# Kernel tuning notes

Hardware: AMD Instinct MI355X
Metric: run time of the kernel (lower is better)

## Reference

```python
import jax, jax.numpy as jnp
import numpy as np

EPS = 1e-5
NUM_GRAPHS = 64


def _linear(x, W, b):
    return x @ W + b


def setup_inputs() -> dict:
    key = jax.random.key(0)
    ks = jax.random.split(key, 32)
    N, E, IN, EF, H, ED, T, L, C = 25000, 400000, 128, 16, 32, 32, 4, 2, 1
    F = H            # F_in (divide_input=False)
    Fo = H // T      # F_out per tower

    def w(k, shape):
        return jax.random.normal(k, shape, jnp.float32) / np.sqrt(shape[-2])

    inp = {
        'x': jax.random.normal(ks[0], (N, IN), jnp.float32),
        'edge_attr': jax.random.normal(ks[1], (E, EF), jnp.float32),
        'edge_weight': jax.random.uniform(ks[2], (E,), jnp.float32),
        'edge_index': jax.random.randint(ks[3], (2, E), 0, N),
        'batch': jnp.sort(jax.random.randint(ks[4], (N,), 0, NUM_GRAPHS)),
        'node_W': w(ks[5], (IN, H)), 'node_b': jnp.zeros((H,), jnp.float32),
        'edge_W': w(ks[6], (EF, ED)), 'edge_b': jnp.zeros((ED,), jnp.float32),
        'enc_W': w(ks[7], (L, ED, F)), 'enc_b': jnp.zeros((L, F), jnp.float32),
        'pre_W': w(ks[8], (L, T, 3 * F, F)), 'pre_b': jnp.zeros((L, T, F), jnp.float32),
        'post_W': w(ks[9], (L, T, 13 * F, Fo)), 'post_b': jnp.zeros((L, T, Fo), jnp.float32),
        'lin_W': w(ks[10], (L, H, H)), 'lin_b': jnp.zeros((L, H), jnp.float32),
        'bn_g': jnp.ones((L, H), jnp.float32), 'bn_b': jnp.zeros((L, H), jnp.float32),
        'mlp_W1': w(ks[11], (H, H)), 'mlp_b1': jnp.zeros((H,), jnp.float32),
        'mlp_W2': w(ks[12], (H, H // 2)), 'mlp_b2': jnp.zeros((H // 2,), jnp.float32),
        'mlp_W3': w(ks[13], (H // 2, C)), 'mlp_b3': jnp.zeros((C,), jnp.float32),
    }
    return inp


def reference(x, edge_attr, edge_weight, node_W, node_b, edge_W, edge_b,
              enc_W, enc_b, pre_W, pre_b, post_W, post_b, lin_W, lin_b,
              bn_g, bn_b, mlp_W1, mlp_b1, mlp_W2, mlp_b2, mlp_W3, mlp_b3,
              edge_index, batch):
    N = x.shape[0]
    L, T = pre_W.shape[0], pre_W.shape[1]
    src, dst = edge_index[0], edge_index[1]

    # degree-based scalers (PNA): avg_deg_log = mean_n log(deg_n + 1)
    deg = jax.ops.segment_sum(jnp.ones((src.shape[0],), x.dtype), dst, num_segments=N)
    avg_deg_log = jnp.mean(jnp.log(deg + 1.0))
    degc = jnp.clip(deg, 1.0)[:, None, None]          # [N,1,1]
    log_deg = jnp.log(degc + 1.0)
    amp = log_deg / avg_deg_log                        # amplification scaler
    att = avg_deg_log / log_deg                        # attenuation scaler
    has_edge = (deg > 0)[:, None, None]

    h = _linear(x, node_W, node_b)                     # node_emb  [N,H]
    e = _linear(edge_attr, edge_W, edge_b)             # edge_emb  [E,ED]

    for l in range(L):
        el = _linear(e, enc_W[l], enc_b[l])            # edge_encoder [E,F]
        m_in = jnp.concatenate([h[dst], h[src], el], axis=-1)      # [E,3F]
        msg = jnp.einsum('ef,tfg->etg', m_in, pre_W[l]) + pre_b[l]  # per-tower pre_nn [E,T,F]
        msg = msg * edge_weight[:, None, None]
        s = jax.ops.segment_sum(msg, dst, num_segments=N)
        s2 = jax.ops.segment_sum(msg * msg, dst, num_segments=N)
        mean = s / degc
        std = jnp.sqrt(jax.nn.relu(s2 / degc - mean * mean) + EPS)
        mn = jnp.where(has_edge, jax.ops.segment_min(msg, dst, num_segments=N), 0.0)
        mx = jnp.where(has_edge, jax.ops.segment_max(msg, dst, num_segments=N), 0.0)
        agg = jnp.concatenate([mean, mn, mx, std], axis=-1)            # [N,T,4F]
        agg = jnp.concatenate([agg, agg * amp, agg * att], axis=-1)    # [N,T,12F]
        out = jnp.concatenate(
            [jnp.broadcast_to(h[:, None, :], (N, T, h.shape[-1])), agg], axis=-1)  # [N,T,13F]
        out = jnp.einsum('ntf,tfg->ntg', out, post_W[l]) + post_b[l]   # post_nn [N,T,Fo]
        out = out.reshape(N, -1) @ lin_W[l] + lin_b[l]                 # [N,H]
        mu = jnp.mean(out, axis=0)
        var = jnp.var(out, axis=0)
        out = (out - mu) / jnp.sqrt(var + EPS) * bn_g[l] + bn_b[l]     # BatchNorm (batch stats)
        h = jax.nn.relu(out)

    g = jax.ops.segment_sum(h, batch, num_segments=NUM_GRAPHS)        # global_add_pool
    g = jax.nn.relu(_linear(g, mlp_W1, mlp_b1))
    g = jax.nn.relu(_linear(g, mlp_W2, mlp_b2))
    return _linear(g, mlp_W3, mlp_b3)
```

## Files before the change

### kernel.cpp

```cpp
#include <hip/hip_runtime.h>

constexpr float kEps = 1e-5f;

__device__ __forceinline__ unsigned short f2bf(float x) {
  unsigned int u = __float_as_uint(x);
  unsigned int r = (u + 0x7fffu + ((u >> 16) & 1u)) >> 16;
  return (unsigned short)r;
}
__device__ __forceinline__ float bflo(unsigned int u) { return __uint_as_float(u << 16); }
__device__ __forceinline__ float bfhi(unsigned int u) { return __uint_as_float(u & 0xffff0000u); }
__device__ __forceinline__ unsigned int packbf(float a, float b) {
  return (unsigned int)f2bf(a) | ((unsigned int)f2bf(b) << 16);
}


__global__ void zero_int2(int* __restrict__ a, int* __restrict__ b, int n) {
  int i = blockIdx.x * blockDim.x + threadIdx.x;
  if (i < n) { a[i] = 0; b[i] = 0; }
}

__global__ void hist_kernel(const int* __restrict__ dst, int* __restrict__ deg, int E) {
  int e = blockIdx.x * blockDim.x + threadIdx.x;
  if (e < E) atomicAdd(&deg[dst[e]], 1);
}

__global__ void scan1_kernel(const int* __restrict__ deg, int* __restrict__ off,
                             int* __restrict__ part, int N) {
  __shared__ int sm[1024];
  int i = blockIdx.x * 1024 + threadIdx.x;
  int v = (i < N) ? deg[i] : 0;
  sm[threadIdx.x] = v;
  __syncthreads();
  for (int o = 1; o < 1024; o <<= 1) {
    int t = (threadIdx.x >= o) ? sm[threadIdx.x - o] : 0;
    __syncthreads();
    sm[threadIdx.x] += t;
    __syncthreads();
  }
  if (i < N) off[i] = sm[threadIdx.x] - v;
  if (threadIdx.x == 1023) part[blockIdx.x] = sm[1023];
}

__global__ void scan2_kernel(int* __restrict__ part, int* __restrict__ off, int nb, int N) {
  if (threadIdx.x == 0) {
    int run = 0;
    for (int b = 0; b < nb; b++) { int p = part[b]; part[b] = run; run += p; }
    off[N] = run;
  }
}

__global__ void scan3_kernel(int* __restrict__ off, const int* __restrict__ part, int N) {
  int i = blockIdx.x * 1024 + threadIdx.x;
  if (i < N) off[i] += part[blockIdx.x];
}

__global__ void fill_kernel(const int* __restrict__ src, const int* __restrict__ dst,
                            const float* __restrict__ ew, const int* __restrict__ off,
                            int* __restrict__ cnt, int* __restrict__ edg,
                            int* __restrict__ srcs, float* __restrict__ ews, int E) {
  int e = blockIdx.x * blockDim.x + threadIdx.x;
  if (e < E) {
    int d = dst[e];
    int slot = off[d] + atomicAdd(&cnt[d], 1);
    edg[slot] = e;
    srcs[slot] = src[e];
    ews[slot] = ew[e];
  }
}

__global__ void egather_kernel(const int* __restrict__ edg, const float4* __restrict__ eattr4,
                               float4* __restrict__ eattrg4, int E4) {
  int i = blockIdx.x * blockDim.x + threadIdx.x;
  if (i < E4) {
    int slot = i >> 2, quad = i & 3;
    int e = edg[slot];
    eattrg4[i] = eattr4[e * 4 + quad];
  }
}

__global__ void adl_kernel(const int* __restrict__ deg, float* __restrict__ adl, int N) {
  __shared__ float sm[1024];
  float s = 0.f;
  for (int n = threadIdx.x; n < N; n += 1024) s += logf((float)deg[n] + 1.f);
  sm[threadIdx.x] = s;
  __syncthreads();
  for (int o = 512; o > 0; o >>= 1) {
    if (threadIdx.x < o) sm[threadIdx.x] += sm[threadIdx.x + o];
    __syncthreads();
  }
  if (threadIdx.x == 0) adl[0] = sm[0];
}

__global__ void node_emb_kernel(const float* __restrict__ x, const float* __restrict__ W,
                                const float* __restrict__ b, float* __restrict__ h, int N) {
  int n = blockIdx.x * 8 + (threadIdx.x >> 5);
  int j = threadIdx.x & 31;
  if (n >= N) return;
  float acc = b[j];
  const float4* x4 = (const float4*)(x + (size_t)n * 128);
#pragma unroll
  for (int q = 0; q < 32; q++) {
    float4 v = x4[q];
    acc += v.x * W[(4 * q + 0) * 32 + j];
    acc += v.y * W[(4 * q + 1) * 32 + j];
    acc += v.z * W[(4 * q + 2) * 32 + j];
    acc += v.w * W[(4 * q + 3) * 32 + j];
  }
  h[n * 32 + j] = acc;
}

__global__ void fuse_kernel(const float* __restrict__ edge_W, const float* __restrict__ edge_b,
                            const float* __restrict__ enc_W, const float* __restrict__ enc_b,
                            const float* __restrict__ pre_W, const float* __restrict__ pre_b,
                            float* __restrict__ Wf, float* __restrict__ bf) {
  __shared__ float tW[2][16][32];
  __shared__ float tb[2][32];
  int tid = threadIdx.x;
  for (int i = tid; i < 1024; i += 256) {
    int l = i >> 9, r = (i >> 5) & 15, c = i & 31;
    float s = 0.f;
    for (int k = 0; k < 32; k++) s += edge_W[r * 32 + k] * enc_W[(l * 32 + k) * 32 + c];
    tW[l][r][c] = s;
  }
  for (int i = tid; i < 64; i += 256) {
    int l = i >> 5, c = i & 31;
    float s = enc_b[l * 32 + c];
    for (int k = 0; k < 32; k++) s += edge_b[k] * enc_W[(l * 32 + k) * 32 + c];
    tb[l][c] = s;
  }
  __syncthreads();
  for (int i = tid; i < 4096; i += 256) {
    int l = i >> 11, t = (i >> 9) & 3, r = (i >> 5) & 15, c = i & 31;
    float s = 0.f;
    for (int k = 0; k < 32; k++) s += tW[l][r][k] * pre_W[((l * 4 + t) * 96 + 64 + k) * 32 + c];
    Wf[i] = s;
  }
  for (int i = tid; i < 256; i += 256) {
    int l = i >> 7, t = (i >> 5) & 3, c = i & 31;
    float s = pre_b[(l * 4 + t) * 32 + c];
    for (int k = 0; k < 32; k++) s += tb[l][k] * pre_W[((l * 4 + t) * 96 + 64 + k) * 32 + c];
    bf[i] = s;
  }
}

__global__ __launch_bounds__(256) void prep_kernel(
    const float* __restrict__ h, const float* __restrict__ preW,
    const float* __restrict__ bfv, unsigned short* __restrict__ qB,
    unsigned short* __restrict__ AB, float* __restrict__ bn, int N) {
  if (blockIdx.x == 0 && threadIdx.x < 64) bn[threadIdx.x] = 0.f;
  __shared__ float hs[16][32];
  int tid = threadIdx.x;
  int c = tid & 127, half = tid >> 7;
  int t = c >> 5, g = c & 31;
  float ws[32], wd[32];
  {
    const float* pS = preW + (t * 96 + 32) * 32 + g;
    const float* pD = preW + (t * 96) * 32 + g;
#pragma unroll
    for (int k = 0; k < 32; k++) { ws[k] = pS[k * 32]; wd[k] = pD[k * 32]; }
  }
  float bc = bfv[c];
  int base = blockIdx.x * 16;
  for (int i = tid; i < 512; i += 256) {
    int nn = i >> 5;
    hs[nn][i & 31] = (base + nn < N) ? h[(size_t)(base + nn) * 32 + (i & 31)] : 0.f;
  }
  __syncthreads();
#pragma unroll
  for (int nn = 0; nn < 8; ++nn) {
    int nl = half + 2 * nn;
    int n = base + nl;
    if (n >= N) continue;
    float qa = 0.f, Aa = bc;
#pragma unroll
    for (int k = 0; k < 32; k++) {
      float hk = hs[nl][k];
      qa = fmaf(hk, ws[k], qa);
      Aa = fmaf(hk, wd[k], Aa);
    }
    qB[(size_t)n * 128 + c] = f2bf(qa);
    AB[(size_t)n * 128 + c] = f2bf(Aa);
  }
}

#define FOLD8(F0, F1, VA, VB, O)                                           \
  F0 = fmaf(VA.x, wfa[O + 0], F0); F1 = fmaf(VA.x, wfb[O + 0], F1);        \
  F0 = fmaf(VA.y, wfa[O + 1], F0); F1 = fmaf(VA.y, wfb[O + 1], F1);        \
  F0 = fmaf(VA.z, wfa[O + 2], F0); F1 = fmaf(VA.z, wfb[O + 2], F1);        \
  F0 = fmaf(VA.w, wfa[O + 3], F0); F1 = fmaf(VA.w, wfb[O + 3], F1);        \
  F0 = fmaf(VB.x, wfa[O + 4], F0); F1 = fmaf(VB.x, wfb[O + 4], F1);        \
  F0 = fmaf(VB.y, wfa[O + 5], F0); F1 = fmaf(VB.y, wfb[O + 5], F1);        \
  F0 = fmaf(VB.z, wfa[O + 6], F0); F1 = fmaf(VB.z, wfb[O + 6], F1);        \
  F0 = fmaf(VB.w, wfa[O + 7], F0); F1 = fmaf(VB.w, wfb[O + 7], F1);

#define STATACC(V0, V1)                                                    \
  s0a += V0; sq0 = fmaf(V0, V0, sq0); mn0 = fminf(mn0, V0); mx0 = fmaxf(mx0, V0); \
  s1a += V1; sq1 = fmaf(V1, V1, sq1); mn1 = fminf(mn1, V1); mx1 = fmaxf(mx1, V1);

__global__ __launch_bounds__(256, 4) void agg3_kernel(
    const unsigned int* __restrict__ qB, const unsigned int* __restrict__ AB,
    const int* __restrict__ coff, const int* __restrict__ srcs,
    const float* __restrict__ ews, const float* __restrict__ eattrg,
    const float* __restrict__ Wf, unsigned int* __restrict__ stats, int N) {
  int lane = threadIdx.x & 63;
  int n = (blockIdx.x * blockDim.x + threadIdx.x) >> 6;
  if (n >= N) return;
  int t = lane >> 4, g0 = (2 * lane) & 31;
  float wfa[16], wfb[16];
  {
    const float* p = Wf + t * 512 + g0;
#pragma unroll
    for (int k = 0; k < 16; k++) { wfa[k] = p[k * 32]; wfb[k] = p[k * 32 + 1]; }
  }
  unsigned int au = AB[(size_t)n * 64 + lane];
  float a0 = bflo(au), a1 = bfhi(au);
  int beg = coff[n], end = coff[n + 1];
  int dg = end - beg;
  float s0a = 0.f, s1a = 0.f, sq0 = 0.f, sq1 = 0.f;
  float mn0 = 1e30f, mn1 = 1e30f, mx0 = -1e30f, mx1 = -1e30f;

  int i = beg;
  int sc0 = 0, sc1 = 0, sc2 = 0, sc3 = 0;
  if (i + 4 <= end) { sc0 = srcs[i]; sc1 = srcs[i + 1]; sc2 = srcs[i + 2]; sc3 = srcs[i + 3]; }
  for (; i + 4 <= end; i += 4) {
    unsigned int q0 = qB[(size_t)sc0 * 64 + lane];
    unsigned int q1 = qB[(size_t)sc1 * 64 + lane];
    unsigned int q2 = qB[(size_t)sc2 * 64 + lane];
    unsigned int q3 = qB[(size_t)sc3 * 64 + lane];
    float w0 = ews[i], w1 = ews[i + 1], w2 = ews[i + 2], w3 = ews[i + 3];
    const float4* ep = (const float4*)(eattrg + (size_t)i * 16);
    if (i + 8 <= end) { sc0 = srcs[i + 4]; sc1 = srcs[i + 5]; sc2 = srcs[i + 6]; sc3 = srcs[i + 7]; }
    float f00 = 0.f, f10 = 0.f, f01 = 0.f, f11 = 0.f;
    float f02 = 0.f, f12 = 0.f, f03 = 0.f, f13 = 0.f;
    {
      float4 aA = ep[0], aB = ep[1], bA = ep[4], bB = ep[5];
      float4 cA = ep[8], cB = ep[9], dA = ep[12], dB = ep[13];
      FOLD8(f00, f10, aA, aB, 0)
      FOLD8(f01, f11, bA, bB, 0)
      FOLD8(f02, f12, cA, cB, 0)
      FOLD8(f03, f13, dA, dB, 0)
    }
    {
      float4 aA = ep[2], aB = ep[3], bA = ep[6], bB = ep[7];
      float4 cA = ep[10], cB = ep[11], dA = ep[14], dB = ep[15];
      FOLD8(f00, f10, aA, aB, 8)
      FOLD8(f01, f11, bA, bB, 8)
      FOLD8(f02, f12, cA, cB, 8)
      FOLD8(f03, f13, dA, dB, 8)
    }
    float v0, v1;
    v0 = (a0 + bflo(q0) + f00) * w0; v1 = (a1 + bfhi(q0) + f10) * w0; STATACC(v0, v1)
    v0 = (a0 + bflo(q1) + f01) * w1; v1 = (a1 + bfhi(q1) + f11) * w1; STATACC(v0, v1)
    v0 = (a0 + bflo(q2) + f02) * w2; v1 = (a1 + bfhi(q2) + f12) * w2; STATACC(v0, v1)
    v0 = (a0 + bflo(q3) + f03) * w3; v1 = (a1 + bfhi(q3) + f13) * w3; STATACC(v0, v1)
  }
  for (; i < end; ++i) {
    int s = srcs[i];
    unsigned int q = qB[(size_t)s * 64 + lane];
    float w = ews[i];
    const float4* ep = (const float4*)(eattrg + (size_t)i * 16);
    float4 aA = ep[0], aB = ep[1], cA = ep[2], cB = ep[3];
    float f0 = 0.f, f1 = 0.f;
    FOLD8(f0, f1, aA, aB, 0)
    FOLD8(f0, f1, cA, cB, 8)
    float v0 = (a0 + bflo(q) + f0) * w;
    float v1 = (a1 + bfhi(q) + f1) * w;
    STATACC(v0, v1)
  }
  if (dg == 0) { mn0 = 0.f; mx0 = 0.f; mn1 = 0.f; mx1 = 0.f; }
  float inv = 1.f / (float)(dg > 0 ? dg : 1);
  float mean0 = s0a * inv, mean1 = s1a * inv;
  float sd0 = sqrtf(fmaxf(sq0 * inv - mean0 * mean0, 0.f) + kEps);
  float sd1 = sqrtf(fmaxf(sq1 * inv - mean1 * mean1, 0.f) + kEps);
  unsigned int* sp = stats + (size_t)n * 256;
  sp[0 * 64 + lane] = packbf(mean0, mean1);
  sp[1 * 64 + lane] = packbf(mn0, mn1);
  sp[2 * 64 + lane] = packbf(mx0, mx1);
  sp[3 * 64 + lane] = packbf(sd0, sd1);
}

__global__ __launch_bounds__(256) void post_kernel(
    const float* __restrict__ h, const unsigned int* __restrict__ stats,
    const int* __restrict__ coff, const float* __restrict__ adl,
    const float* __restrict__ postW, const float* __restrict__ postB,
    const float* __restrict__ linW, const float* __restrict__ linB,
    float* __restrict__ pre, float* __restrict__ bn, int N) {
  __shared__ unsigned int pwp[208 * 32];
  __shared__ unsigned int stu[4][256];
  __shared__ float red[8][32];
  int tid = threadIdx.x;
  for (int i = tid; i < 6656; i += 256) {
    int r = i >> 5, cc = i & 31, tP = cc >> 3, gq = cc & 7;
    float lo = postW[tP * 3328 + (2 * r) * 8 + gq];
    float hi = postW[tP * 3328 + (2 * r + 1) * 8 + gq];
    pwp[i] = packbf(lo, hi);
  }
  __syncthreads();

  int wave = tid >> 6, lane = tid & 63;
  int c = lane & 31, hh = lane >> 5;
  int tP = c >> 3;
  float adN = adl[0];
  float bs = 0.f, bq = 0.f;

  for (int n = blockIdx.x * 4 + wave; n < N; n += gridDim.x * 4) {
    {
      uint4 su = ((const uint4*)stats)[(size_t)n * 64 + lane];
      ((uint4*)stu[wave])[lane] = su;
    }
    int dg = coff[n + 1] - coff[n];
    float degc = (float)(dg > 0 ? dg : 1);
    float ad = adN / (float)N;
    float ld = logf(degc + 1.f);
    float amp = ld / ad, att = ad / ld;

    float acc = (hh == 0) ? postB[tP * 8 + (c & 7)] : 0.f;
    const float4* h4 = (const float4*)(h + (size_t)n * 32);
#pragma unroll
    for (int q4 = 0; q4 < 4; q4++) {
      float4 hv = h4[hh * 4 + q4];
      int r0 = hh * 8 + q4 * 2;
      unsigned int u0 = pwp[r0 * 32 + c], u1 = pwp[(r0 + 1) * 32 + c];
      acc = fmaf(hv.x, bflo(u0), acc);
      acc = fmaf(hv.y, bfhi(u0), acc);
      acc = fmaf(hv.z, bflo(u1), acc);
      acc = fmaf(hv.w, bfhi(u1), acc);
    }
#pragma unroll 8
    for (int jj = 0; jj < 32; jj++) {
      int sIdx = hh * 2 + (jj >> 4);
      unsigned int sv = stu[wave][sIdx * 64 + tP * 16 + (jj & 15)];
      float v0 = bflo(sv), v1 = bfhi(sv);
      int rm = 16 + hh * 32 + jj, ra = 80 + hh * 32 + jj, rt = 144 + hh * 32 + jj;
      unsigned int um = pwp[rm * 32 + c];
      unsigned int ua = pwp[ra * 32 + c];
      unsigned int ut = pwp[rt * 32 + c];
      float w0 = bflo(um); w0 = fmaf(amp, bflo(ua), w0); w0 = fmaf(att, bflo(ut), w0);
      float w1 = bfhi(um); w1 = fmaf(amp, bfhi(ua), w1); w1 = fmaf(att, bfhi(ut), w1);
      acc = fmaf(v0, w0, acc);
      acc = fmaf(v1, w1, acc);
    }
    acc += __shfl_xor(acc, 32);
    float o = linB[c];
#pragma unroll
    for (int k = 0; k < 32; k++) {
      float a = __shfl(acc, k);
      o = fmaf(a, linW[k * 32 + c], o);
    }
    if (lane < 32) {
      pre[(size_t)n * 32 + c] = o;
      bs += o;
      bq = fmaf(o, o, bq);
    }
  }

  __syncthreads();
  if (lane < 32) {
    red[wave * 2 + 0][c] = bs;
    red[wave * 2 + 1][c] = bq;
  }
  __syncthreads();
  if (tid < 64) {
    int which = tid >> 5, cc = tid & 31;
    float s = red[0 * 2 + which][cc] + red[1 * 2 + which][cc] +
              red[2 * 2 + which][cc] + red[3 * 2 + which][cc];
    atomicAdd(&bn[which * 32 + cc], s);
  }
}

__global__ void bn_apply_kernel(const float* __restrict__ pre, const float* __restrict__ bn,
                                const float* __restrict__ gamma, const float* __restrict__ beta,
                                float* __restrict__ h, int N) {
  int i = blockIdx.x * 256 + threadIdx.x;
  if (i >= N * 32) return;
  int j = i & 31;
  float invN = 1.f / (float)N;
  float mu = bn[j] * invN;
  float var = bn[32 + j] * invN - mu * mu;
  float is = rsqrtf(var + kEps);
  float v = (pre[i] - mu) * is * gamma[j] + beta[j];
  h[i] = fmaxf(v, 0.f);
}


__device__ __forceinline__ int lower_bound_dev(const int* a, int n, int key) {
  int lo = 0, hi = n;
  while (lo < hi) {
    int m = (lo + hi) >> 1;
    if (a[m] < key) lo = m + 1; else hi = m;
  }
  return lo;
}

__global__ void pool_kernel(const float* __restrict__ h, const int* __restrict__ batch,
                            float* __restrict__ gp, int N) {
  int gi = blockIdx.x;
  int lo = lower_bound_dev(batch, N, gi);
  int hi = lower_bound_dev(batch, N, gi + 1);
  __shared__ float part[8][32];
  int j = threadIdx.x & 31, ch = threadIdx.x >> 5;
  float s = 0.f;
  for (int n = lo + ch; n < hi; n += 8) s += h[(size_t)n * 32 + j];
  part[ch][j] = s;
  __syncthreads();
  if (threadIdx.x < 32) {
    float t = 0.f;
    for (int c2 = 0; c2 < 8; c2++) t += part[c2][j];
    gp[gi * 32 + j] = t;
  }
}

__global__ void mlp_kernel(const float* __restrict__ gp,
                           const float* __restrict__ W1, const float* __restrict__ b1,
                           const float* __restrict__ W2, const float* __restrict__ b2,
                           const float* __restrict__ W3, const float* __restrict__ b3,
                           float* __restrict__ out) {
  __shared__ float g1[64 * 32];
  __shared__ float g2[64 * 16];
  int tid = threadIdx.x;
  for (int i = tid; i < 2048; i += 256) {
    int r = i >> 5, c = i & 31;
    float s = b1[c];
    for (int k = 0; k < 32; k++) s += gp[r * 32 + k] * W1[k * 32 + c];
    g1[i] = fmaxf(s, 0.f);
  }
  __syncthreads();
  for (int i = tid; i < 1024; i += 256) {
    int r = i >> 4, c = i & 15;
    float s = b2[c];
    for (int k = 0; k < 32; k++) s += g1[r * 32 + k] * W2[k * 16 + c];
    g2[i] = fmaxf(s, 0.f);
  }
  __syncthreads();
  if (tid < 64) {
    float s = b3[0];
    for (int k = 0; k < 16; k++) s += g2[tid * 16 + k] * W3[k];
    out[tid] = s;
  }
}


extern "C" void kernel_launch(void* const* d_in, const int* in_sizes, int n_in,
                              void* d_out, int out_size, void* d_ws, size_t ws_size,
                              hipStream_t stream) {
  (void)n_in; (void)out_size; (void)ws_size;
  const float* x     = (const float*)d_in[0];
  const float* eattr = (const float*)d_in[1];
  const float* ew    = (const float*)d_in[2];
  const int*   eidx  = (const int*)d_in[3];
  const int*   batch = (const int*)d_in[4];
  const float* nodeW = (const float*)d_in[5];
  const float* nodeB = (const float*)d_in[6];
  const float* edgeW = (const float*)d_in[7];
  const float* edgeB = (const float*)d_in[8];
  const float* encW  = (const float*)d_in[9];
  const float* encB  = (const float*)d_in[10];
  const float* preW  = (const float*)d_in[11];
  const float* preB  = (const float*)d_in[12];
  const float* postW = (const float*)d_in[13];
  const float* postB = (const float*)d_in[14];
  const float* linW  = (const float*)d_in[15];
  const float* linB  = (const float*)d_in[16];
  const float* bnG   = (const float*)d_in[17];
  const float* bnB   = (const float*)d_in[18];
  const float* W1    = (const float*)d_in[19];
  const float* b1    = (const float*)d_in[20];
  const float* W2    = (const float*)d_in[21];
  const float* b2    = (const float*)d_in[22];
  const float* W3    = (const float*)d_in[23];
  const float* b3    = (const float*)d_in[24];
  float* out = (float*)d_out;

  int N = in_sizes[0] / 128;
  int E = in_sizes[2];
  const int* srcp = eidx;
  const int* dstp = eidx + E;

  char* wsb = (char*)d_ws;
  size_t woff = 0;
  auto alloc = [&](size_t bytes) -> void* {
    void* p = (void*)(wsb + woff);
    woff += (bytes + 255) & ~(size_t)255;
    return p;
  };
  int* deg   = (int*)alloc((size_t)N * 4);
  int* cnt   = (int*)alloc((size_t)N * 4);
  int* coff  = (int*)alloc((size_t)(N + 1) * 4);
  int* part  = (int*)alloc(64 * 4);
  int* edg   = (int*)alloc((size_t)E * 4);
  int* srcs  = (int*)alloc((size_t)E * 4);
  float* ews = (float*)alloc((size_t)E * 4);
  float* eattrg = (float*)alloc((size_t)E * 16 * 4);
  float* h    = (float*)alloc((size_t)N * 32 * 4);
  float* pre  = (float*)alloc((size_t)N * 32 * 4);
  float* adl  = (float*)alloc(256);
  float* bn   = (float*)alloc(64 * 4);
  float* gp   = (float*)alloc(64 * 32 * 4);
  float* WfB  = (float*)alloc(2 * 4 * 16 * 32 * 4);
  float* bfB  = (float*)alloc(2 * 4 * 32 * 4);
  unsigned short* qB  = (unsigned short*)alloc((size_t)N * 128 * 2);
  unsigned short* AB  = (unsigned short*)alloc((size_t)N * 128 * 2);
  unsigned int* stats = (unsigned int*)alloc((size_t)N * 256 * 4);

  int nb = (N + 1023) / 1024;
  zero_int2<<<(N + 255) / 256, 256, 0, stream>>>(deg, cnt, N);
  hist_kernel<<<(E + 255) / 256, 256, 0, stream>>>(dstp, deg, E);
  scan1_kernel<<<nb, 1024, 0, stream>>>(deg, coff, part, N);
  scan2_kernel<<<1, 64, 0, stream>>>(part, coff, nb, N);
  scan3_kernel<<<nb, 1024, 0, stream>>>(coff, part, N);
  fill_kernel<<<(E + 255) / 256, 256, 0, stream>>>(srcp, dstp, ew, coff, cnt, edg, srcs, ews, E);
  egather_kernel<<<(E * 4 + 255) / 256, 256, 0, stream>>>(edg, (const float4*)eattr,
                                                          (float4*)eattrg, E * 4);
  adl_kernel<<<1, 1024, 0, stream>>>(deg, adl, N);
  node_emb_kernel<<<(N + 7) / 8, 256, 0, stream>>>(x, nodeW, nodeB, h, N);
  fuse_kernel<<<1, 256, 0, stream>>>(edgeW, edgeB, encW, encB, preW, preB, WfB, bfB);

  for (int l = 0; l < 2; l++) {
    prep_kernel<<<(N + 15) / 16, 256, 0, stream>>>(
        h, preW + (size_t)l * 12288, bfB + (size_t)l * 128, qB, AB, bn, N);
    agg3_kernel<<<(N + 3) / 4, 256, 0, stream>>>(
        (const unsigned int*)qB, (const unsigned int*)AB, coff, srcs, ews,
        eattrg, WfB + (size_t)l * 2048, stats, N);
    post_kernel<<<1280, 256, 0, stream>>>(
        h, stats, coff, adl,
        postW + (size_t)l * 13312, postB + (size_t)l * 32,
        linW + (size_t)l * 1024, linB + (size_t)l * 32, pre, bn, N);
    bn_apply_kernel<<<(N * 32 + 255) / 256, 256, 0, stream>>>(pre, bn, bnG + (size_t)l * 32,
                                                              bnB + (size_t)l * 32, h, N);
  }
  pool_kernel<<<64, 256, 0, stream>>>(h, batch, gp, N);
  mlp_kernel<<<1, 256, 0, stream>>>(gp, W1, b1, W2, b2, W3, b3, out);
}
```

Measured before the change: 453.4 us.

## Fuse BN into prep and pool, split edge aggregation across waves, repack post weights

Merges the edge-attribute gather into the CSR fill kernel and folds the BatchNorm apply into the next layer's prep kernel and into the final pooling kernel, which removes separate launches and extra passes over node features. The aggregation kernel now assigns two waves to each node, each covering half of the edge list, and merges their partial statistics through shared memory to add parallelism for high-degree nodes. The post kernel stores its mean, amp and att weights together as uint4 so that one LDS load replaces three. The layer loop is unrolled and the BN statistic buffers are zeroed once at the start, which adds a block-wide barrier in aggregation and duplicates some normalisation arithmetic.

```diff
diff --git a/kernel.cpp b/kernel.cpp
--- a/kernel.cpp
+++ b/kernel.cpp
@@ -14,9 +14,11 @@
 }
 
 
-__global__ void zero_int2(int* __restrict__ a, int* __restrict__ b, int n) {
+__global__ void zero_kernel(int* __restrict__ a, int* __restrict__ b,
+                            float* __restrict__ bnb, int n) {
   int i = blockIdx.x * blockDim.x + threadIdx.x;
   if (i < n) { a[i] = 0; b[i] = 0; }
+  if (i < 128) bnb[i] = 0.f;
 }
 
 __global__ void hist_kernel(const int* __restrict__ dst, int* __restrict__ deg, int E) {
@@ -55,26 +57,22 @@
 }
 
 __global__ void fill_kernel(const int* __restrict__ src, const int* __restrict__ dst,
-                            const float* __restrict__ ew, const int* __restrict__ off,
-                            int* __restrict__ cnt, int* __restrict__ edg,
-                            int* __restrict__ srcs, float* __restrict__ ews, int E) {
+                            const float* __restrict__ ew, const float4* __restrict__ eattr4,
+                            const int* __restrict__ off, int* __restrict__ cnt,
+                            int* __restrict__ srcs, float* __restrict__ ews,
+                            float4* __restrict__ eattrg4, int E) {
   int e = blockIdx.x * blockDim.x + threadIdx.x;
   if (e < E) {
     int d = dst[e];
     int slot = off[d] + atomicAdd(&cnt[d], 1);
-    edg[slot] = e;
     srcs[slot] = src[e];
     ews[slot] = ew[e];
-  }
-}
-
-__global__ void egather_kernel(const int* __restrict__ edg, const float4* __restrict__ eattr4,
-                               float4* __restrict__ eattrg4, int E4) {
-  int i = blockIdx.x * blockDim.x + threadIdx.x;
-  if (i < E4) {
-    int slot = i >> 2, quad = i & 3;
-    int e = edg[slot];
-    eattrg4[i] = eattr4[e * 4 + quad];
+    float4 a = eattr4[e * 4 + 0], b = eattr4[e * 4 + 1];
+    float4 c = eattr4[e * 4 + 2], q = eattr4[e * 4 + 3];
+    eattrg4[(size_t)slot * 4 + 0] = a;
+    eattrg4[(size_t)slot * 4 + 1] = b;
+    eattrg4[(size_t)slot * 4 + 2] = c;
+    eattrg4[(size_t)slot * 4 + 3] = q;
   }
 }
 
@@ -146,8 +144,7 @@
 __global__ __launch_bounds__(256) void prep_kernel(
     const float* __restrict__ h, const float* __restrict__ preW,
     const float* __restrict__ bfv, unsigned short* __restrict__ qB,
-    unsigned short* __restrict__ AB, float* __restrict__ bn, int N) {
-  if (blockIdx.x == 0 && threadIdx.x < 64) bn[threadIdx.x] = 0.f;
+    unsigned short* __restrict__ AB, int N) {
   __shared__ float hs[16][32];
   int tid = threadIdx.x;
   int c = tid & 127, half = tid >> 7;
@@ -165,6 +162,57 @@
     int nn = i >> 5;
     hs[nn][i & 31] = (base + nn < N) ? h[(size_t)(base + nn) * 32 + (i & 31)] : 0.f;
   }
+  __syncthreads();
+#pragma unroll
+  for (int nn = 0; nn < 8; ++nn) {
+    int nl = half + 2 * nn;
+    int n = base + nl;
+    if (n >= N) continue;
+    float qa = 0.f, Aa = bc;
+#pragma unroll
+    for (int k = 0; k < 32; k++) {
+      float hk = hs[nl][k];
+      qa = fmaf(hk, ws[k], qa);
+      Aa = fmaf(hk, wd[k], Aa);
+    }
+    qB[(size_t)n * 128 + c] = f2bf(qa);
+    AB[(size_t)n * 128 + c] = f2bf(Aa);
+  }
+}
+
+__global__ __launch_bounds__(256) void bnprep_kernel(
+    const float* __restrict__ pre, const float* __restrict__ bnv,
+    const float* __restrict__ gamma, const float* __restrict__ beta,
+    const float* __restrict__ preW, const float* __restrict__ bfv,
+    float* __restrict__ h, unsigned short* __restrict__ qB,
+    unsigned short* __restrict__ AB, int N) {
+  __shared__ float hs[16][32];
+  int tid = threadIdx.x;
+  int base = blockIdx.x * 16;
+  float invN = 1.f / (float)N;
+  for (int idx = tid; idx < 512; idx += 256) {
+    int nn = idx >> 5, j = idx & 31;
+    int n = base + nn;
+    float v = 0.f;
+    if (n < N) {
+      float mu = bnv[j] * invN;
+      float var = bnv[32 + j] * invN - mu * mu;
+      float is = rsqrtf(var + kEps);
+      v = fmaxf((pre[(size_t)n * 32 + j] - mu) * is * gamma[j] + beta[j], 0.f);
+      h[(size_t)n * 32 + j] = v;
+    }
+    hs[nn][j] = v;
+  }
+  int c = tid & 127, half = tid >> 7;
+  int t = c >> 5, g = c & 31;
+  float ws[32], wd[32];
+  {
+    const float* pS = preW + (t * 96 + 32) * 32 + g;
+    const float* pD = preW + (t * 96) * 32 + g;
+#pragma unroll
+    for (int k = 0; k < 32; k++) { ws[k] = pS[k * 32]; wd[k] = pD[k * 32]; }
+  }
+  float bc = bfv[c];
   __syncthreads();
 #pragma unroll
   for (int nn = 0; nn < 8; ++nn) {
@@ -197,14 +245,16 @@
   s0a += V0; sq0 = fmaf(V0, V0, sq0); mn0 = fminf(mn0, V0); mx0 = fmaxf(mx0, V0); \
   s1a += V1; sq1 = fmaf(V1, V1, sq1); mn1 = fminf(mn1, V1); mx1 = fmaxf(mx1, V1);
 
-__global__ __launch_bounds__(256, 4) void agg3_kernel(
+__global__ __launch_bounds__(256, 4) void agg6_kernel(
     const unsigned int* __restrict__ qB, const unsigned int* __restrict__ AB,
     const int* __restrict__ coff, const int* __restrict__ srcs,
     const float* __restrict__ ews, const float* __restrict__ eattrg,
     const float* __restrict__ Wf, unsigned int* __restrict__ stats, int N) {
-  int lane = threadIdx.x & 63;
-  int n = (blockIdx.x * blockDim.x + threadIdx.x) >> 6;
-  if (n >= N) return;
+  __shared__ float comb[2][64][8];
+  int tid = threadIdx.x, wave = tid >> 6, lane = tid & 63;
+  int pairIdx = wave >> 1, half = wave & 1;
+  int n = blockIdx.x * 2 + pairIdx;
+  bool valid = (n < N);
   int t = lane >> 4, g0 = (2 * lane) & 31;
   float wfa[16], wfb[16];
   {
@@ -212,24 +262,31 @@
 #pragma unroll
     for (int k = 0; k < 16; k++) { wfa[k] = p[k * 32]; wfb[k] = p[k * 32 + 1]; }
   }
-  unsigned int au = AB[(size_t)n * 64 + lane];
-  float a0 = bflo(au), a1 = bfhi(au);
-  int beg = coff[n], end = coff[n + 1];
-  int dg = end - beg;
+  float a0 = 0.f, a1 = 0.f;
+  int lo = 0, hi = 0, dg = 0;
+  if (valid) {
+    unsigned int au = AB[(size_t)n * 64 + lane];
+    a0 = bflo(au); a1 = bfhi(au);
+    int beg = coff[n], end = coff[n + 1];
+    dg = end - beg;
+    int mid = beg + ((dg + 1) >> 1);
+    lo = half ? mid : beg;
+    hi = half ? end : mid;
+  }
   float s0a = 0.f, s1a = 0.f, sq0 = 0.f, sq1 = 0.f;
   float mn0 = 1e30f, mn1 = 1e30f, mx0 = -1e30f, mx1 = -1e30f;
 
-  int i = beg;
+  int i = lo;
   int sc0 = 0, sc1 = 0, sc2 = 0, sc3 = 0;
-  if (i + 4 <= end) { sc0 = srcs[i]; sc1 = srcs[i + 1]; sc2 = srcs[i + 2]; sc3 = srcs[i + 3]; }
-  for (; i + 4 <= end; i += 4) {
+  if (i + 4 <= hi) { sc0 = srcs[i]; sc1 = srcs[i + 1]; sc2 = srcs[i + 2]; sc3 = srcs[i + 3]; }
+  for (; i + 4 <= hi; i += 4) {
     unsigned int q0 = qB[(size_t)sc0 * 64 + lane];
     unsigned int q1 = qB[(size_t)sc1 * 64 + lane];
     unsigned int q2 = qB[(size_t)sc2 * 64 + lane];
     unsigned int q3 = qB[(size_t)sc3 * 64 + lane];
     float w0 = ews[i], w1 = ews[i + 1], w2 = ews[i + 2], w3 = ews[i + 3];
     const float4* ep = (const float4*)(eattrg + (size_t)i * 16);
-    if (i + 8 <= end) { sc0 = srcs[i + 4]; sc1 = srcs[i + 5]; sc2 = srcs[i + 6]; sc3 = srcs[i + 7]; }
+    if (i + 8 <= hi) { sc0 = srcs[i + 4]; sc1 = srcs[i + 5]; sc2 = srcs[i + 6]; sc3 = srcs[i + 7]; }
     float f00 = 0.f, f10 = 0.f, f01 = 0.f, f11 = 0.f;
     float f02 = 0.f, f12 = 0.f, f03 = 0.f, f13 = 0.f;
     {
@@ -254,7 +311,7 @@
     v0 = (a0 + bflo(q2) + f02) * w2; v1 = (a1 + bfhi(q2) + f12) * w2; STATACC(v0, v1)
     v0 = (a0 + bflo(q3) + f03) * w3; v1 = (a1 + bfhi(q3) + f13) * w3; STATACC(v0, v1)
   }
-  for (; i < end; ++i) {
+  for (; i < hi; ++i) {
     int s = srcs[i];
     unsigned int q = qB[(size_t)s * 64 + lane];
     float w = ews[i];
@@ -267,16 +324,29 @@
     float v1 = (a1 + bfhi(q) + f1) * w;
     STATACC(v0, v1)
   }
-  if (dg == 0) { mn0 = 0.f; mx0 = 0.f; mn1 = 0.f; mx1 = 0.f; }
-  float inv = 1.f / (float)(dg > 0 ? dg : 1);
-  float mean0 = s0a * inv, mean1 = s1a * inv;
-  float sd0 = sqrtf(fmaxf(sq0 * inv - mean0 * mean0, 0.f) + kEps);
-  float sd1 = sqrtf(fmaxf(sq1 * inv - mean1 * mean1, 0.f) + kEps);
-  unsigned int* sp = stats + (size_t)n * 256;
-  sp[0 * 64 + lane] = packbf(mean0, mean1);
-  sp[1 * 64 + lane] = packbf(mn0, mn1);
-  sp[2 * 64 + lane] = packbf(mx0, mx1);
-  sp[3 * 64 + lane] = packbf(sd0, sd1);
+
+  if (half) {
+    float* cb = comb[pairIdx][lane];
+    cb[0] = s0a; cb[1] = s1a; cb[2] = sq0; cb[3] = sq1;
+    cb[4] = mn0; cb[5] = mn1; cb[6] = mx0; cb[7] = mx1;
+  }
+  __syncthreads();
+  if (valid && !half) {
+    const float* cb = comb[pairIdx][lane];
+    s0a += cb[0]; s1a += cb[1]; sq0 += cb[2]; sq1 += cb[3];
+    mn0 = fminf(mn0, cb[4]); mn1 = fminf(mn1, cb[5]);
+    mx0 = fmaxf(mx0, cb[6]); mx1 = fmaxf(mx1, cb[7]);
+    if (dg == 0) { mn0 = 0.f; mx0 = 0.f; mn1 = 0.f; mx1 = 0.f; }
+    float inv = 1.f / (float)(dg > 0 ? dg : 1);
+    float mean0 = s0a * inv, mean1 = s1a * inv;
+    float sd0 = sqrtf(fmaxf(sq0 * inv - mean0 * mean0, 0.f) + kEps);
+    float sd1 = sqrtf(fmaxf(sq1 * inv - mean1 * mean1, 0.f) + kEps);
+    unsigned int* sp = stats + (size_t)n * 256;
+    sp[0 * 64 + lane] = packbf(mean0, mean1);
+    sp[1 * 64 + lane] = packbf(mn0, mn1);
+    sp[2 * 64 + lane] = packbf(mx0, mx1);
+    sp[3 * 64 + lane] = packbf(sd0, sd1);
+  }
 }
 
 __global__ __launch_bounds__(256) void post_kernel(
@@ -285,15 +355,26 @@
     const float* __restrict__ postW, const float* __restrict__ postB,
     const float* __restrict__ linW, const float* __restrict__ linB,
     float* __restrict__ pre, float* __restrict__ bn, int N) {
-  __shared__ unsigned int pwp[208 * 32];
+  __shared__ unsigned int ph[512];
+  __shared__ uint4 pq[2048];
   __shared__ unsigned int stu[4][256];
   __shared__ float red[8][32];
   int tid = threadIdx.x;
-  for (int i = tid; i < 6656; i += 256) {
+  for (int i = tid; i < 512; i += 256) {
     int r = i >> 5, cc = i & 31, tP = cc >> 3, gq = cc & 7;
-    float lo = postW[tP * 3328 + (2 * r) * 8 + gq];
-    float hi = postW[tP * 3328 + (2 * r + 1) * 8 + gq];
-    pwp[i] = packbf(lo, hi);
+    ph[i] = packbf(postW[tP * 3328 + (2 * r) * 8 + gq],
+                   postW[tP * 3328 + (2 * r + 1) * 8 + gq]);
+  }
+  for (int i = tid; i < 2048; i += 256) {
+    int rr = i >> 5, cc = i & 31, tP = cc >> 3, gq = cc & 7;
+    int stat = rr >> 4, jp = rr & 15;
+    int fb = 32 + stat * 32 + 2 * jp;
+    uint4 w;
+    w.x = packbf(postW[tP * 3328 + fb * 8 + gq], postW[tP * 3328 + (fb + 1) * 8 + gq]);
+    w.y = packbf(postW[tP * 3328 + (fb + 128) * 8 + gq], postW[tP * 3328 + (fb + 129) * 8 + gq]);
+    w.z = packbf(postW[tP * 3328 + (fb + 256) * 8 + gq], postW[tP * 3328 + (fb + 257) * 8 + gq]);
+    w.w = 0u;
+    pq[i] = w;
   }
   __syncthreads();
 
@@ -320,7 +401,7 @@
     for (int q4 = 0; q4 < 4; q4++) {
       float4 hv = h4[hh * 4 + q4];
       int r0 = hh * 8 + q4 * 2;
-      unsigned int u0 = pwp[r0 * 32 + c], u1 = pwp[(r0 + 1) * 32 + c];
+      unsigned int u0 = ph[r0 * 32 + c], u1 = ph[(r0 + 1) * 32 + c];
       acc = fmaf(hv.x, bflo(u0), acc);
       acc = fmaf(hv.y, bfhi(u0), acc);
       acc = fmaf(hv.z, bflo(u1), acc);
@@ -329,14 +410,12 @@
 #pragma unroll 8
     for (int jj = 0; jj < 32; jj++) {
       int sIdx = hh * 2 + (jj >> 4);
-      unsigned int sv = stu[wave][sIdx * 64 + tP * 16 + (jj & 15)];
+      int jp = jj & 15;
+      unsigned int sv = stu[wave][sIdx * 64 + tP * 16 + jp];
       float v0 = bflo(sv), v1 = bfhi(sv);
-      int rm = 16 + hh * 32 + jj, ra = 80 + hh * 32 + jj, rt = 144 + hh * 32 + jj;
-      unsigned int um = pwp[rm * 32 + c];
-      unsigned int ua = pwp[ra * 32 + c];
-      unsigned int ut = pwp[rt * 32 + c];
-      float w0 = bflo(um); w0 = fmaf(amp, bflo(ua), w0); w0 = fmaf(att, bflo(ut), w0);
-      float w1 = bfhi(um); w1 = fmaf(amp, bfhi(ua), w1); w1 = fmaf(att, bfhi(ut), w1);
+      uint4 wq = pq[(sIdx * 16 + jp) * 32 + c];
+      float w0 = bflo(wq.x); w0 = fmaf(amp, bflo(wq.y), w0); w0 = fmaf(att, bflo(wq.z), w0);
+      float w1 = bfhi(wq.x); w1 = fmaf(amp, bfhi(wq.y), w1); w1 = fmaf(att, bfhi(wq.z), w1);
       acc = fmaf(v0, w0, acc);
       acc = fmaf(v1, w1, acc);
     }
@@ -368,20 +447,6 @@
   }
 }
 
-__global__ void bn_apply_kernel(const float* __restrict__ pre, const float* __restrict__ bn,
-                                const float* __restrict__ gamma, const float* __restrict__ beta,
-                                float* __restrict__ h, int N) {
-  int i = blockIdx.x * 256 + threadIdx.x;
-  if (i >= N * 32) return;
-  int j = i & 31;
-  float invN = 1.f / (float)N;
-  float mu = bn[j] * invN;
-  float var = bn[32 + j] * invN - mu * mu;
-  float is = rsqrtf(var + kEps);
-  float v = (pre[i] - mu) * is * gamma[j] + beta[j];
-  h[i] = fmaxf(v, 0.f);
-}
-
 
 __device__ __forceinline__ int lower_bound_dev(const int* a, int n, int key) {
   int lo = 0, hi = n;
@@ -392,15 +457,22 @@
   return lo;
 }
 
-__global__ void pool_kernel(const float* __restrict__ h, const int* __restrict__ batch,
-                            float* __restrict__ gp, int N) {
+__global__ void pool2_kernel(const float* __restrict__ pre, const float* __restrict__ bnv,
+                             const float* __restrict__ gamma, const float* __restrict__ beta,
+                             const int* __restrict__ batch, float* __restrict__ gp, int N) {
   int gi = blockIdx.x;
   int lo = lower_bound_dev(batch, N, gi);
   int hi = lower_bound_dev(batch, N, gi + 1);
   __shared__ float part[8][32];
   int j = threadIdx.x & 31, ch = threadIdx.x >> 5;
+  float invN = 1.f / (float)N;
+  float mu = bnv[j] * invN;
+  float var = bnv[32 + j] * invN - mu * mu;
+  float is = rsqrtf(var + kEps);
+  float gm = gamma[j], bt = beta[j];
   float s = 0.f;
-  for (int n = lo + ch; n < hi; n += 8) s += h[(size_t)n * 32 + j];
+  for (int n = lo + ch; n < hi; n += 8)
+    s += fmaxf((pre[(size_t)n * 32 + j] - mu) * is * gm + bt, 0.f);
   part[ch][j] = s;
   __syncthreads();
   if (threadIdx.x < 32) {
@@ -487,14 +559,13 @@
   int* cnt   = (int*)alloc((size_t)N * 4);
   int* coff  = (int*)alloc((size_t)(N + 1) * 4);
   int* part  = (int*)alloc(64 * 4);
-  int* edg   = (int*)alloc((size_t)E * 4);
   int* srcs  = (int*)alloc((size_t)E * 4);
   float* ews = (float*)alloc((size_t)E * 4);
   float* eattrg = (float*)alloc((size_t)E * 16 * 4);
   float* h    = (float*)alloc((size_t)N * 32 * 4);
   float* pre  = (float*)alloc((size_t)N * 32 * 4);
   float* adl  = (float*)alloc(256);
-  float* bn   = (float*)alloc(64 * 4);
+  float* bnbuf = (float*)alloc(2 * 64 * 4);
   float* gp   = (float*)alloc(64 * 32 * 4);
   float* WfB  = (float*)alloc(2 * 4 * 16 * 32 * 4);
   float* bfB  = (float*)alloc(2 * 4 * 32 * 4);
@@ -503,31 +574,33 @@
   unsigned int* stats = (unsigned int*)alloc((size_t)N * 256 * 4);
 
   int nb = (N + 1023) / 1024;
-  zero_int2<<<(N + 255) / 256, 256, 0, stream>>>(deg, cnt, N);
+  zero_kernel<<<(N + 255) / 256, 256, 0, stream>>>(deg, cnt, bnbuf, N);
   hist_kernel<<<(E + 255) / 256, 256, 0, stream>>>(dstp, deg, E);
   scan1_kernel<<<nb, 1024, 0, stream>>>(deg, coff, part, N);
   scan2_kernel<<<1, 64, 0, stream>>>(part, coff, nb, N);
   scan3_kernel<<<nb, 1024, 0, stream>>>(coff, part, N);
-  fill_kernel<<<(E + 255) / 256, 256, 0, stream>>>(srcp, dstp, ew, coff, cnt, edg, srcs, ews, E);
-  egather_kernel<<<(E * 4 + 255) / 256, 256, 0, stream>>>(edg, (const float4*)eattr,
-                                                          (float4*)eattrg, E * 4);
+  fill_kernel<<<(E + 255) / 256, 256, 0, stream>>>(srcp, dstp, ew, (const float4*)eattr,
+                                                   coff, cnt, srcs, ews, (float4*)eattrg, E);
   adl_kernel<<<1, 1024, 0, stream>>>(deg, adl, N);
   node_emb_kernel<<<(N + 7) / 8, 256, 0, stream>>>(x, nodeW, nodeB, h, N);
   fuse_kernel<<<1, 256, 0, stream>>>(edgeW, edgeB, encW, encB, preW, preB, WfB, bfB);
 
-  for (int l = 0; l < 2; l++) {
-    prep_kernel<<<(N + 15) / 16, 256, 0, stream>>>(
-        h, preW + (size_t)l * 12288, bfB + (size_t)l * 128, qB, AB, bn, N);
-    agg3_kernel<<<(N + 3) / 4, 256, 0, stream>>>(
-        (const unsigned int*)qB, (const unsigned int*)AB, coff, srcs, ews,
-        eattrg, WfB + (size_t)l * 2048, stats, N);
-    post_kernel<<<1280, 256, 0, stream>>>(
-        h, stats, coff, adl,
-        postW + (size_t)l * 13312, postB + (size_t)l * 32,
-        linW + (size_t)l * 1024, linB + (size_t)l * 32, pre, bn, N);
-    bn_apply_kernel<<<(N * 32 + 255) / 256, 256, 0, stream>>>(pre, bn, bnG + (size_t)l * 32,
-                                                              bnB + (size_t)l * 32, h, N);
-  }
-  pool_kernel<<<64, 256, 0, stream>>>(h, batch, gp, N);
+  int grid_a = (N + 1) / 2;
+
+  prep_kernel<<<(N + 15) / 16, 256, 0, stream>>>(h, preW, bfB, qB, AB, N);
+  agg6_kernel<<<grid_a, 256, 0, stream>>>(
+      (const unsigned int*)qB, (const unsigned int*)AB, coff, srcs, ews,
+      eattrg, WfB, stats, N);
+  post_kernel<<<1280, 256, 0, stream>>>(
+      h, stats, coff, adl, postW, postB, linW, linB, pre, bnbuf, N);
+  bnprep_kernel<<<(N + 15) / 16, 256, 0, stream>>>(
+      pre, bnbuf, bnG, bnB, preW + 12288, bfB + 128, h, qB, AB, N);
+  agg6_kernel<<<grid_a, 256, 0, stream>>>(
+      (const unsigned int*)qB, (const unsigned int*)AB, coff, srcs, ews,
+      eattrg, WfB + 2048, stats, N);
+  post_kernel<<<1280, 256, 0, stream>>>(
+      h, stats, coff, adl, postW + 13312, postB + 32, linW + 1024, linB + 32,
+      pre, bnbuf + 64, N);
+  pool2_kernel<<<64, 256, 0, stream>>>(pre, bnbuf + 64, bnG + 32, bnB + 32, batch, gp, N);
   mlp_kernel<<<1, 256, 0, stream>>>(gp, W1, b1, W2, b2, W3, b3, out);
 }
```

Result: slower. 480.2 us (+5.9%).
